# Performance work log

Measured on AMD Instinct MI355X. Metric: run time of the kernel, lower is better.

## Reference

```python
import jax, jax.numpy as jnp
import numpy as np

N_NODES = 50000
N_EDGES = 800000
IN_CH = 128
MEAN_SIZE = 128
VAR_SIZE = 128


def setup_inputs() -> dict:
    key = jax.random.key(0)
    k_x, k_e, k_wm, k_wv = jax.random.split(key, 4)
    x = jax.random.normal(k_x, (N_NODES, IN_CH), dtype=jnp.float32)
    edge_index = jax.random.randint(k_e, (2, N_EDGES), 0, N_NODES, dtype=jnp.int32)
    # torch Linear(2*C, M, bias=False) weight has shape [M, 2*C]
    s = 1.0 / np.sqrt(2 * IN_CH)
    w_mean = jax.random.uniform(k_wm, (MEAN_SIZE, 2 * IN_CH), jnp.float32, -s, s)
    w_var = jax.random.uniform(k_wv, (VAR_SIZE, 2 * IN_CH), jnp.float32, -s, s)
    return {"x": x, "edge_index": edge_index, "w_mean": w_mean, "w_var": w_var}


def reference(x, edge_index, w_mean, w_var):
    row, col = edge_index[0], edge_index[1]
    x_row = x[row]  # [E, C]
    x_col = x[col]  # [E, C]
    # cat([x_row, x_col], 1) @ W.T  ==  x_row @ W[:, :C].T + x_col @ W[:, C:].T
    C = x.shape[1]
    maps_mean = jnp.einsum('ec,mc->em', x_row, w_mean[:, :C]) + \
                jnp.einsum('ec,mc->em', x_col, w_mean[:, C:])
    maps_var = jnp.einsum('ec,vc->ev', x_row, w_var[:, :C]) + \
               jnp.einsum('ec,vc->ev', x_col, w_var[:, C:])
    return (maps_mean, maps_var)
```

## Files before the change

kernel.cpp:

```cpp
#include <hip/hip_runtime.h>
#include <hip/hip_bf16.h>

#define NODES 50000
#define EDGES 800000
#define CH 128
#define NCOL 512
#define MPAD 50048
#define EPW 8

typedef __attribute__((ext_vector_type(8))) __bf16 bf16x8;
typedef __attribute__((ext_vector_type(4))) float f32x4;
typedef unsigned long long u64;

static __device__ __forceinline__ unsigned short f2bf(float f) {
    union { float f; unsigned u; } v; v.f = f;
    unsigned r = v.u + 0x7FFFu + ((v.u >> 16) & 1u);
    return (unsigned short)(r >> 16);
}
static __device__ __forceinline__ float bf2f(unsigned short h) {
    union { unsigned u; float f; } v; v.u = ((unsigned)h) << 16;
    return v.f;
}

__global__ void k_cvt_x(const float* __restrict__ x, unsigned short* __restrict__ xb) {
    int i = blockIdx.x * blockDim.x + threadIdx.x;
    if (i >= MPAD * CH / 4) return;
    int base = i << 2;
    unsigned short s0 = 0, s1 = 0, s2 = 0, s3 = 0;
    if (base < NODES * CH) {
        const f32x4 v = *reinterpret_cast<const f32x4*>(x + base);
        s0 = f2bf(v[0]); s1 = f2bf(v[1]); s2 = f2bf(v[2]); s3 = f2bf(v[3]);
    }
    u64 p = (u64)s0 | ((u64)s1 << 16) | ((u64)s2 << 32) | ((u64)s3 << 48);
    *reinterpret_cast<u64*>(xb + base) = p;
}

__global__ void k_pack_w(const float* __restrict__ wm, const float* __restrict__ wv,
                         unsigned short* __restrict__ wb) {
    int i = blockIdx.x * blockDim.x + threadIdx.x;
    if (i >= NCOL * CH) return;
    int n = i >> 7, k = i & 127;
    float v;
    if (n < 128)      v = wm[n * 256 + k];
    else if (n < 256) v = wv[(n - 128) * 256 + k];
    else if (n < 384) v = wm[(n - 256) * 256 + 128 + k];
    else              v = wv[(n - 384) * 256 + 128 + k];
    wb[i] = f2bf(v);
}

__global__ __launch_bounds__(256) void k_gemm(const unsigned short* __restrict__ xb,
                                              const unsigned short* __restrict__ wb,
                                              unsigned short* __restrict__ th) {
    const int lane = threadIdx.x & 63;
    const int wave = threadIdx.x >> 6;
    const int rowbase = blockIdx.x * 128 + (wave >> 1) * 64;
    const int colbase = blockIdx.y * 128 + (wave & 1) * 64;
    const int lr = lane & 15;
    const int kg = lane >> 4;
    f32x4 acc[4][4] = {};
#pragma unroll
    for (int ks = 0; ks < 4; ++ks) {
        const int k = ks * 32 + kg * 8;
        bf16x8 af[4], bfr[4];
#pragma unroll
        for (int a = 0; a < 4; ++a)
            af[a] = *reinterpret_cast<const bf16x8*>(xb + (size_t)(rowbase + a * 16 + lr) * CH + k);
#pragma unroll
        for (int b = 0; b < 4; ++b)
            bfr[b] = *reinterpret_cast<const bf16x8*>(wb + (size_t)(colbase + b * 16 + lr) * CH + k);
#pragma unroll
        for (int a = 0; a < 4; ++a)
#pragma unroll
            for (int b = 0; b < 4; ++b)
                acc[a][b] = __builtin_amdgcn_mfma_f32_16x16x32_bf16(af[a], bfr[b], acc[a][b], 0, 0, 0);
    }
    const int crow = (lane >> 4) * 4;
    const int ccol = lane & 15;
#pragma unroll
    for (int a = 0; a < 4; ++a)
#pragma unroll
        for (int b = 0; b < 4; ++b)
#pragma unroll
            for (int j = 0; j < 4; ++j) {
                int row = rowbase + a * 16 + crow + j;
                int col = colbase + b * 16 + ccol;
                th[(size_t)row * NCOL + col] = f2bf(acc[a][b][j]);
            }
}

__global__ __launch_bounds__(256) void k_edges(const int* __restrict__ ei,
                                               const unsigned short* __restrict__ th,
                                               float* __restrict__ out) {
    const int wave = threadIdx.x >> 6;
    const int lane = threadIdx.x & 63;
    const int half = lane >> 5;
    const int l = lane & 31;
    const int ebase = (blockIdx.x * 4 + wave) * EPW;

    int rr[EPW], cc[EPW];
#pragma unroll
    for (int i = 0; i < EPW; ++i) {
        rr[i] = ei[ebase + i];
        cc[i] = ei[EDGES + ebase + i];
    }
    u64 pa[EPW], pb[EPW];
#pragma unroll
    for (int i = 0; i < EPW; ++i) {
        pa[i] = *reinterpret_cast<const u64*>(th + (size_t)rr[i] * NCOL + half * 128 + l * 4);
        pb[i] = *reinterpret_cast<const u64*>(th + (size_t)cc[i] * NCOL + 256 + half * 128 + l * 4);
    }
    const size_t obase = (size_t)half * ((size_t)EDGES * 128) + (size_t)l * 4;
#pragma unroll
    for (int i = 0; i < EPW; ++i) {
        f32x4 s;
        s[0] = bf2f((unsigned short)pa[i])         + bf2f((unsigned short)pb[i]);
        s[1] = bf2f((unsigned short)(pa[i] >> 16)) + bf2f((unsigned short)(pb[i] >> 16));
        s[2] = bf2f((unsigned short)(pa[i] >> 32)) + bf2f((unsigned short)(pb[i] >> 32));
        s[3] = bf2f((unsigned short)(pa[i] >> 48)) + bf2f((unsigned short)(pb[i] >> 48));
        __builtin_nontemporal_store(
            s, reinterpret_cast<f32x4*>(out + obase + (size_t)(ebase + i) * 128));
    }
}

__global__ void k_naive(const float* __restrict__ x, const int* __restrict__ ei,
                        const float* __restrict__ wm, const float* __restrict__ wv,
                        float* __restrict__ out) {
    __shared__ float xs[256];
    int e = blockIdx.x;
    int t = threadIdx.x;
    int r = ei[e], c = ei[EDGES + e];
    xs[t] = (t < 128) ? x[(size_t)r * 128 + t] : x[(size_t)c * 128 + (t - 128)];
    __syncthreads();
    const float* w = (t < 128) ? (wm + (size_t)t * 256) : (wv + (size_t)(t - 128) * 256);
    float acc = 0.f;
#pragma unroll 8
    for (int k = 0; k < 256; ++k) acc = fmaf(xs[k], w[k], acc);
    size_t ooff = (t < 128) ? ((size_t)e * 128 + t)
                            : ((size_t)EDGES * 128 + (size_t)e * 128 + (t - 128));
    out[ooff] = acc;
}

extern "C" void kernel_launch(void* const* d_in, const int* in_sizes, int n_in,
                              void* d_out, int out_size, void* d_ws, size_t ws_size,
                              hipStream_t stream) {
    const float* x  = (const float*)d_in[0];
    const int*   ei = (const int*)d_in[1];
    const float* wm = (const float*)d_in[2];
    const float* wv = (const float*)d_in[3];
    float* out = (float*)d_out;

    const size_t xb_b = (size_t)MPAD * CH * 2;
    const size_t wb_b = (size_t)NCOL * CH * 2;
    const size_t th_b = (size_t)MPAD * NCOL * 2;

    if (ws_size < xb_b + wb_b + th_b) {
        k_naive<<<EDGES, 256, 0, stream>>>(x, ei, wm, wv, out);
        return;
    }

    unsigned short* xb  = (unsigned short*)d_ws;
    unsigned short* wb  = (unsigned short*)((char*)d_ws + xb_b);
    unsigned short* tab = (unsigned short*)((char*)d_ws + xb_b + wb_b);

    k_cvt_x<<<(MPAD * CH / 4 + 255) / 256, 256, 0, stream>>>(x, xb);
    k_pack_w<<<(NCOL * CH + 255) / 256, 256, 0, stream>>>(wm, wv, wb);
    dim3 g(MPAD / 128, NCOL / 128);
    k_gemm<<<g, 256, 0, stream>>>(xb, wb, tab);
    k_edges<<<EDGES / (4 * EPW), 256, 0, stream>>>(ei, tab, out);
}
```

Measured before the change: 273.2 us.

## Bin edges by row node range before gather to improve table locality

```diff
diff --git a/kernel.cpp b/kernel.cpp
--- a/kernel.cpp
+++ b/kernel.cpp
@@ -7,6 +7,9 @@
 #define NCOL 512
 #define MPAD 50048
 #define EPW 8
+#define NB 196
+#define BINBLK 256
+#define CHUNK 3125
 
 typedef __attribute__((ext_vector_type(8))) __bf16 bf16x8;
 typedef __attribute__((ext_vector_type(4))) float f32x4;
@@ -88,6 +91,92 @@
             }
 }
 
+__global__ void k_zero(unsigned* __restrict__ hist) {
+    if (threadIdx.x < 256) hist[threadIdx.x] = 0;
+}
+
+__global__ __launch_bounds__(256) void k_binA(const int* __restrict__ ei,
+                                              unsigned* __restrict__ hist,
+                                              unsigned* __restrict__ blockOff) {
+    __shared__ unsigned h[NB];
+    for (int t = threadIdx.x; t < NB; t += 256) h[t] = 0;
+    __syncthreads();
+    const int base = blockIdx.x * CHUNK;
+    for (int i = threadIdx.x; i < CHUNK; i += 256)
+        atomicAdd(&h[((unsigned)ei[base + i]) >> 8], 1u);
+    __syncthreads();
+    for (int t = threadIdx.x; t < NB; t += 256)
+        blockOff[blockIdx.x * NB + t] = atomicAdd(&hist[t], h[t]);
+}
+
+__global__ void k_scan(const unsigned* __restrict__ hist, unsigned* __restrict__ basearr) {
+    __shared__ unsigned v[256];
+    int t = threadIdx.x;
+    unsigned mine = (t < NB) ? hist[t] : 0;
+    v[t] = mine;
+    __syncthreads();
+    for (int off = 1; off < 256; off <<= 1) {
+        unsigned x = (t >= off) ? v[t - off] : 0;
+        __syncthreads();
+        v[t] += x;
+        __syncthreads();
+    }
+    if (t < NB) basearr[t] = v[t] - mine;
+}
+
+__global__ __launch_bounds__(256) void k_binB(const int* __restrict__ ei,
+                                              const unsigned* __restrict__ basearr,
+                                              const unsigned* __restrict__ blockOff,
+                                              u64* __restrict__ binned) {
+    __shared__ unsigned cur[NB];
+    for (int t = threadIdx.x; t < NB; t += 256) cur[t] = 0;
+    __syncthreads();
+    const int base = blockIdx.x * CHUNK;
+    for (int i = threadIdx.x; i < CHUNK; i += 256) {
+        int e = base + i;
+        unsigned r = (unsigned)ei[e];
+        unsigned c = (unsigned)ei[EDGES + e];
+        unsigned b = r >> 8;
+        unsigned rank = atomicAdd(&cur[b], 1u);
+        unsigned pos = basearr[b] + blockOff[blockIdx.x * NB + b] + rank;
+        binned[pos] = (u64)r | ((u64)c << 17) | ((u64)e << 34);
+    }
+}
+
+__global__ __launch_bounds__(256) void k_edges_b(const u64* __restrict__ binned,
+                                                 const unsigned short* __restrict__ th,
+                                                 float* __restrict__ out) {
+    const int wave = threadIdx.x >> 6;
+    const int lane = threadIdx.x & 63;
+    const int half = lane >> 5;
+    const int l = lane & 31;
+    const int ebase = (blockIdx.x * 4 + wave) * EPW;
+
+    u64 rec[EPW];
+#pragma unroll
+    for (int i = 0; i < EPW; ++i) rec[i] = binned[ebase + i];
+    u64 pa[EPW], pb[EPW];
+#pragma unroll
+    for (int i = 0; i < EPW; ++i) {
+        const unsigned r = (unsigned)(rec[i] & 0x1FFFF);
+        const unsigned c = (unsigned)((rec[i] >> 17) & 0x1FFFF);
+        pa[i] = *reinterpret_cast<const u64*>(th + (size_t)r * NCOL + half * 128 + l * 4);
+        pb[i] = *reinterpret_cast<const u64*>(th + (size_t)c * NCOL + 256 + half * 128 + l * 4);
+    }
+    const size_t obase = (size_t)half * ((size_t)EDGES * 128) + (size_t)l * 4;
+#pragma unroll
+    for (int i = 0; i < EPW; ++i) {
+        const unsigned e = (unsigned)(rec[i] >> 34);
+        f32x4 s;
+        s[0] = bf2f((unsigned short)pa[i])         + bf2f((unsigned short)pb[i]);
+        s[1] = bf2f((unsigned short)(pa[i] >> 16)) + bf2f((unsigned short)(pb[i] >> 16));
+        s[2] = bf2f((unsigned short)(pa[i] >> 32)) + bf2f((unsigned short)(pb[i] >> 32));
+        s[3] = bf2f((unsigned short)(pa[i] >> 48)) + bf2f((unsigned short)(pb[i] >> 48));
+        __builtin_nontemporal_store(
+            s, reinterpret_cast<f32x4*>(out + obase + (size_t)e * 128));
+    }
+}
+
 __global__ __launch_bounds__(256) void k_edges(const int* __restrict__ ei,
                                                const unsigned short* __restrict__ th,
                                                float* __restrict__ out) {
@@ -96,13 +185,9 @@
     const int half = lane >> 5;
     const int l = lane & 31;
     const int ebase = (blockIdx.x * 4 + wave) * EPW;
-
     int rr[EPW], cc[EPW];
 #pragma unroll
-    for (int i = 0; i < EPW; ++i) {
-        rr[i] = ei[ebase + i];
-        cc[i] = ei[EDGES + ebase + i];
-    }
+    for (int i = 0; i < EPW; ++i) { rr[i] = ei[ebase + i]; cc[i] = ei[EDGES + ebase + i]; }
     u64 pa[EPW], pb[EPW];
 #pragma unroll
     for (int i = 0; i < EPW; ++i) {
@@ -149,22 +234,43 @@
     const float* wv = (const float*)d_in[3];
     float* out = (float*)d_out;
 
-    const size_t xb_b = (size_t)MPAD * CH * 2;
-    const size_t wb_b = (size_t)NCOL * CH * 2;
-    const size_t th_b = (size_t)MPAD * NCOL * 2;
-
-    if (ws_size < xb_b + wb_b + th_b) {
+    const size_t xb_b   = (size_t)MPAD * CH * 2;
+    const size_t wb_b   = (size_t)NCOL * CH * 2;
+    const size_t th_b   = (size_t)MPAD * NCOL * 2;
+    const size_t hist_b = 1024;
+    const size_t base_b = 1024;
+    const size_t boff_b = (size_t)BINBLK * NB * 4;
+    const size_t bin_b  = (size_t)EDGES * 8;
+
+    const size_t need_tab = xb_b + wb_b + th_b;
+    const size_t need_bin = need_tab + hist_b + base_b + boff_b + bin_b;
+
+    if (ws_size < need_tab) {
         k_naive<<<EDGES, 256, 0, stream>>>(x, ei, wm, wv, out);
         return;
     }
 
-    unsigned short* xb  = (unsigned short*)d_ws;
-    unsigned short* wb  = (unsigned short*)((char*)d_ws + xb_b);
-    unsigned short* tab = (unsigned short*)((char*)d_ws + xb_b + wb_b);
+    char* w0 = (char*)d_ws;
+    unsigned short* xb  = (unsigned short*)w0;
+    unsigned short* wb  = (unsigned short*)(w0 + xb_b);
+    unsigned short* tab = (unsigned short*)(w0 + xb_b + wb_b);
 
     k_cvt_x<<<(MPAD * CH / 4 + 255) / 256, 256, 0, stream>>>(x, xb);
     k_pack_w<<<(NCOL * CH + 255) / 256, 256, 0, stream>>>(wm, wv, wb);
     dim3 g(MPAD / 128, NCOL / 128);
     k_gemm<<<g, 256, 0, stream>>>(xb, wb, tab);
-    k_edges<<<EDGES / (4 * EPW), 256, 0, stream>>>(ei, tab, out);
-}
+
+    if (ws_size >= need_bin) {
+        unsigned* hist    = (unsigned*)(w0 + need_tab);
+        unsigned* basearr = (unsigned*)(w0 + need_tab + hist_b);
+        unsigned* boff    = (unsigned*)(w0 + need_tab + hist_b + base_b);
+        u64*      binned  = (u64*)    (w0 + need_tab + hist_b + base_b + boff_b);
+        k_zero<<<1, 256, 0, stream>>>(hist);
+        k_binA<<<BINBLK, 256, 0, stream>>>(ei, hist, boff);
+        k_scan<<<1, 256, 0, stream>>>(hist, basearr);
+        k_binB<<<BINBLK, 256, 0, stream>>>(ei, basearr, boff, binned);
+        k_edges_b<<<EDGES / (4 * EPW), 256, 0, stream>>>(binned, tab, out);
+    } else {
+        k_edges<<<EDGES / (4 * EPW), 256, 0, stream>>>(ei, tab, out);
+    }
+}
```

Measured after the change: 267.3 us. 2.2% less time.
